# Kernel tuning notes

Hardware: AMD Instinct MI355X
Metric: run time of the kernel (lower is better)

The kernel has to match this reference:

```python
import jax, jax.numpy as jnp
import numpy as np

BATCH = 65536
INPUT_DIM = 256
FIELD_DIM = 32
OUTPUT_DIM = 30


def setup_inputs() -> dict:
    key = jax.random.key(0)
    k1, k2, k3 = jax.random.split(key, 3)
    x = jax.random.normal(k1, (BATCH, INPUT_DIM), dtype=jnp.float32)
    kernel = jax.random.normal(k2, (INPUT_DIM, OUTPUT_DIM), dtype=jnp.float32) * 0.1
    field_weight_matrix = jax.random.normal(k3, (FIELD_DIM, FIELD_DIM), dtype=jnp.float32) * 0.1
    # field_dict[i] = i % FIELD_DIM (matches init_kwargs)
    field_ids = (jnp.arange(INPUT_DIM) % FIELD_DIM).astype(jnp.int32)
    return {"x": x, "kernel": kernel, "field_weight_matrix": field_weight_matrix, "field_ids": field_ids}


def reference(x, kernel, field_weight_matrix, field_ids):
    # Pairwise factor weights: (k_i . k_j) for all i,j  -> [D, D]
    kk = kernel @ kernel.T
    # Field-weight gather: F[field[i], field[j]]  -> [D, D]
    fw = field_weight_matrix[field_ids[:, None], field_ids[None, :]]
    # Only i < j pairs, as in the original double loop
    M = jnp.triu(kk * fw, k=1)
    # out_b = sum_{i<j} x_bi * x_bj * M_ij
    out = jnp.einsum("bi,ij,bj->b", x, M, x)
    return out
```

## Files before the change

### kernel.cpp

```cpp
#include <hip/hip_runtime.h>
#include <stdint.h>
#include <stddef.h>

#define IDIM 256

typedef __attribute__((ext_vector_type(8))) short bf16x8;
typedef __attribute__((ext_vector_type(4))) float f32x4;

__device__ __forceinline__ short f2bf(float f) {
    union { float f; unsigned u; } v; v.f = f;
    unsigned r = v.u + 0x7FFFu + ((v.u >> 16) & 1u);
    return (short)(r >> 16);
}

#define FIOFF 73728
#define FWOFF 74752
#define KOFF  78848
#define LDSZ  95232

#define SWZ(r) ((((r) >> 1) & 3) << 4)

__global__ __launch_bounds__(1024, 4)
void fused_qform(const float* __restrict__ X, const float* __restrict__ K,
                 const float* __restrict__ FW, const int* __restrict__ FI,
                 float* __restrict__ out) {
    __shared__ char lds[LDSZ];
    const int tid  = threadIdx.x;
    const int lane = tid & 63;
    const int wave = tid >> 6;
    const int l15  = lane & 15;
    const int g    = lane >> 4;
    const int wrow = blockIdx.x * 256 + wave * 16;
    const int kbase = g * 8;

    float kv[8];
    {
        const float* kr = K + (size_t)(16 * wave + l15) * 30 + kbase;
        #pragma unroll
        for (int e = 0; e < 8; ++e)
            kv[e] = (kbase + e < 30) ? kr[e] : 0.f;
    }
    if (wave < 4) {
        const char* src = (const char*)FW + wave * 1024 + lane * 16;
        __builtin_amdgcn_global_load_lds(
            (const __attribute__((address_space(1))) unsigned*)src,
            (__attribute__((address_space(3))) unsigned*)(lds + FWOFF + wave * 1024),
            16, 0, 0);
    } else if (wave == 4) {
        const char* src = (const char*)FI + lane * 16;
        __builtin_amdgcn_global_load_lds(
            (const __attribute__((address_space(1))) unsigned*)src,
            (__attribute__((address_space(3))) unsigned*)(lds + FIOFF),
            16, 0, 0);
    }
    __builtin_amdgcn_sched_barrier(0);

    const float* xrow = X + (size_t)(wrow + l15) * IDIM + kbase;
    float4 pa[4], pb[4];
    pa[0] = *(const float4*)(xrow + 0 * 32);
    pb[0] = *(const float4*)(xrow + 0 * 32 + 4);
    pa[1] = *(const float4*)(xrow + 1 * 32);
    pb[1] = *(const float4*)(xrow + 1 * 32 + 4);
    pa[2] = *(const float4*)(xrow + 2 * 32);
    pb[2] = *(const float4*)(xrow + 2 * 32 + 4);
    pa[3] = *(const float4*)(xrow + 3 * 32);
    pb[3] = *(const float4*)(xrow + 3 * 32 + 4);
    __builtin_amdgcn_sched_barrier(0);

    {
        bf16x8 f;
        #pragma unroll
        for (int e = 0; e < 8; ++e) f[e] = f2bf(kv[e]);
        *(bf16x8*)(lds + KOFF + wave * 1024 + lane * 16) = f;
    }
    {
        const int ht = tid >> 7;
        const int r  = (tid >> 3) & 15;
        const int a  = tid & 7;
        const int zb = ((ht * (ht + 1) + (2 * ht + 1)) << 10) + r * 64 + ((a * 4) ^ SWZ(r));
        *(unsigned*)(lds + zb) = 0u;
    }
    asm volatile("s_waitcnt vmcnt(8) lgkmcnt(0)" ::: "memory");
    __builtin_amdgcn_s_barrier();
    asm volatile("" ::: "memory");

    {
        const f32x4 kz = (f32x4){0.f, 0.f, 0.f, 0.f};
        const int* ldsFI = (const int*)(lds + FIOFF);
        const float* ldsFW = (const float*)(lds + FWOFF);

        const int v   = wave >> 1;
        const int par = wave & 1;
        const int tb1 = v;
        const int tb2 = 15 - v;
        const bf16x8 bf1 = *(const bf16x8*)(lds + KOFF + tb1 * 1024 + lane * 16);
        const bf16x8 bf2 = *(const bf16x8*)(lds + KOFF + tb2 * 1024 + lane * 16);
        const int fij1 = ldsFI[16 * tb1 + l15];
        const int fij2 = ldsFI[16 * tb2 + l15];

#define BUILD_TILE(ta, tb, fb, fij) do {                                          \
        const bf16x8 aa = *(const bf16x8*)(lds + KOFF + (ta) * 1024 + lane * 16); \
        f32x4 kk = __builtin_amdgcn_mfma_f32_16x16x32_bf16(aa, fb, kz, 0, 0, 0);  \
        const int tjm = (tb) >> 1;                                                \
        const int mb  = ((tjm * (tjm + 1) + (ta)) << 10);                         \
        const int jb0 = (((tb) & 1) << 5) + 2 * l15;                              \
        const int j   = 16 * (tb) + l15;                                          \
        _Pragma("unroll")                                                         \
        for (int q = 0; q < 4; ++q) {                                             \
            const int i15 = g * 4 + q;                                            \
            const int i   = 16 * (ta) + i15;                                      \
            const float fw = ldsFW[ldsFI[16 * (ta) + i15] * 32 + (fij)];          \
            const float val = (j > i) ? kk[q] * fw : 0.f;                         \
            *(short*)(lds + mb + i15 * 64 + (jb0 ^ SWZ(i15))) = f2bf(val);        \
        }                                                                         \
    } while (0)

        #pragma unroll
        for (int ta = 0; ta < 16; ++ta) {
            if ((ta & 1) == par) {
                if (ta <= tb1) BUILD_TILE(ta, tb1, bf1, fij1);
                if (ta <= tb2) BUILD_TILE(ta, tb2, bf2, fij2);
            }
        }
#undef BUILD_TILE
    }

    asm volatile("s_waitcnt lgkmcnt(0)" ::: "memory");
    __builtin_amdgcn_s_barrier();
    asm volatile("" ::: "memory");

    f32x4 acc[16];
    #pragma unroll
    for (int t = 0; t < 16; ++t) acc[t] = (f32x4){0.f, 0.f, 0.f, 0.f};

    const unsigned laneoff = (unsigned)l15 * 64u + (unsigned)((g * 16) ^ SWZ(l15));

    #pragma unroll
    for (int tj = 0; tj < 8; ++tj) {
        const int s = tj & 3;
        const float4 fa = pa[s], fb = pb[s];
        bf16x8 af;
        af[0] = f2bf(fa.x); af[1] = f2bf(fa.y); af[2] = f2bf(fa.z); af[3] = f2bf(fa.w);
        af[4] = f2bf(fb.x); af[5] = f2bf(fb.y); af[6] = f2bf(fb.z); af[7] = f2bf(fb.w);
        if (tj < 4) {
            pa[s] = *(const float4*)(xrow + (tj + 4) * 32);
            pb[s] = *(const float4*)(xrow + (tj + 4) * 32 + 4);
        }
        #pragma unroll
        for (int ti = 0; ti < 16; ++ti) {
            if (ti <= 2 * tj + 1) {
                const bf16x8 b = *(const bf16x8*)(lds + ((tj * (tj + 1) + ti) << 10) + laneoff);
                acc[ti] = __builtin_amdgcn_mfma_f32_16x16x32_bf16(af, b, acc[ti], 0, 0, 0);
            }
        }
    }

    float psum[4] = {0.f, 0.f, 0.f, 0.f};
    const float* xm = X + (size_t)(wrow + g * 4) * IDIM + l15;
    #pragma unroll
    for (int ti = 0; ti < 16; ++ti) {
        #pragma unroll
        for (int q = 0; q < 4; ++q)
            psum[q] += xm[(size_t)q * IDIM + ti * 16] * acc[ti][q];
    }

    #pragma unroll
    for (int q = 0; q < 4; ++q) {
        float v = psum[q];
        v += __shfl_xor(v, 1, 64);
        v += __shfl_xor(v, 2, 64);
        v += __shfl_xor(v, 4, 64);
        v += __shfl_xor(v, 8, 64);
        psum[q] = v;
    }
    if (l15 == 0) {
        #pragma unroll
        for (int q = 0; q < 4; ++q)
            out[wrow + g * 4 + q] = psum[q];
    }
}

extern "C" void kernel_launch(void* const* d_in, const int* in_sizes, int n_in,
                              void* d_out, int out_size, void* d_ws, size_t ws_size,
                              hipStream_t stream) {
    const float* X  = (const float*)d_in[0];
    const float* K  = (const float*)d_in[1];
    const float* FW = (const float*)d_in[2];
    const int*   FI = (const int*)d_in[3];
    const int batch = in_sizes[0] / IDIM;
    fused_qform<<<dim3(batch / 256), dim3(1024), 0, stream>>>(X, K, FW, FI, (float*)d_out);
}
```

Measured before the change: 108.7 us.

## Halve block size and alias K staging buffer into M tile region

The block shrinks from 1024 to 512 threads covering 128 rows, and the bf16 K staging buffer now aliases the last M tile row instead of having its own region. LDS per block drops so two blocks can share a CU. Building M is reorganised: waves 0-6 build the tiles for columns 0-13, then after an extra barrier each wave builds the column 14/15 tiles from K values already held in registers. The cost is that every block rebuilds the whole M matrix for half as many rows, plus one more barrier.

```diff
diff --git a/kernel.cpp b/kernel.cpp
--- a/kernel.cpp
+++ b/kernel.cpp
@@ -15,12 +15,12 @@
 
 #define FIOFF 73728
 #define FWOFF 74752
-#define KOFF  78848
-#define LDSZ  95232
+#define LDSZ  78848
 
 #define SWZ(r) ((((r) >> 1) & 3) << 4)
-
-__global__ __launch_bounds__(1024, 4)
+#define KBT(t) (lds + (56 + (t)) * 1024 + lane * 16)
+
+__global__ __launch_bounds__(512, 4)
 void fused_qform(const float* __restrict__ X, const float* __restrict__ K,
                  const float* __restrict__ FW, const int* __restrict__ FI,
                  float* __restrict__ out) {
@@ -30,15 +30,18 @@
     const int wave = tid >> 6;
     const int l15  = lane & 15;
     const int g    = lane >> 4;
-    const int wrow = blockIdx.x * 256 + wave * 16;
+    const int wrow = blockIdx.x * 128 + wave * 16;
     const int kbase = g * 8;
 
-    float kv[8];
+    float kv0[8], kv1[8];
     {
-        const float* kr = K + (size_t)(16 * wave + l15) * 30 + kbase;
-        #pragma unroll
-        for (int e = 0; e < 8; ++e)
-            kv[e] = (kbase + e < 30) ? kr[e] : 0.f;
+        const float* kr0 = K + (size_t)(16 * (2 * wave)     + l15) * 30 + kbase;
+        const float* kr1 = K + (size_t)(16 * (2 * wave + 1) + l15) * 30 + kbase;
+        #pragma unroll
+        for (int e = 0; e < 8; ++e) {
+            kv0[e] = (kbase + e < 30) ? kr0[e] : 0.f;
+            kv1[e] = (kbase + e < 30) ? kr1[e] : 0.f;
+        }
     }
     if (wave < 4) {
         const char* src = (const char*)FW + wave * 1024 + lane * 16;
@@ -68,38 +71,30 @@
     __builtin_amdgcn_sched_barrier(0);
 
     {
-        bf16x8 f;
-        #pragma unroll
-        for (int e = 0; e < 8; ++e) f[e] = f2bf(kv[e]);
-        *(bf16x8*)(lds + KOFF + wave * 1024 + lane * 16) = f;
+        bf16x8 f0, f1;
+        #pragma unroll
+        for (int e = 0; e < 8; ++e) { f0[e] = f2bf(kv0[e]); f1[e] = f2bf(kv1[e]); }
+        *(bf16x8*)KBT(2 * wave)     = f0;
+        *(bf16x8*)KBT(2 * wave + 1) = f1;
     }
     {
-        const int ht = tid >> 7;
-        const int r  = (tid >> 3) & 15;
-        const int a  = tid & 7;
-        const int zb = ((ht * (ht + 1) + (2 * ht + 1)) << 10) + r * 64 + ((a * 4) ^ SWZ(r));
-        *(unsigned*)(lds + zb) = 0u;
+        const int ht = tid >> 6;
+        if (ht < 7) {
+            const int r  = (lane >> 2) & 15;
+            const int a  = lane & 3;
+            const int zb = ((ht * (ht + 1) + (2 * ht + 1)) << 10) + r * 64 + ((a * 8) ^ SWZ(r));
+            *(unsigned long long*)(lds + zb) = 0ull;
+        }
     }
     asm volatile("s_waitcnt vmcnt(8) lgkmcnt(0)" ::: "memory");
     __builtin_amdgcn_s_barrier();
     asm volatile("" ::: "memory");
 
-    {
-        const f32x4 kz = (f32x4){0.f, 0.f, 0.f, 0.f};
-        const int* ldsFI = (const int*)(lds + FIOFF);
-        const float* ldsFW = (const float*)(lds + FWOFF);
-
-        const int v   = wave >> 1;
-        const int par = wave & 1;
-        const int tb1 = v;
-        const int tb2 = 15 - v;
-        const bf16x8 bf1 = *(const bf16x8*)(lds + KOFF + tb1 * 1024 + lane * 16);
-        const bf16x8 bf2 = *(const bf16x8*)(lds + KOFF + tb2 * 1024 + lane * 16);
-        const int fij1 = ldsFI[16 * tb1 + l15];
-        const int fij2 = ldsFI[16 * tb2 + l15];
-
-#define BUILD_TILE(ta, tb, fb, fij) do {                                          \
-        const bf16x8 aa = *(const bf16x8*)(lds + KOFF + (ta) * 1024 + lane * 16); \
+    const f32x4 kz = (f32x4){0.f, 0.f, 0.f, 0.f};
+    const int* ldsFI = (const int*)(lds + FIOFF);
+    const float* ldsFW = (const float*)(lds + FWOFF);
+
+#define BUILD_TILE_R(ta, tb, aa, fb, fij) do {                                    \
         f32x4 kk = __builtin_amdgcn_mfma_f32_16x16x32_bf16(aa, fb, kz, 0, 0, 0);  \
         const int tjm = (tb) >> 1;                                                \
         const int mb  = ((tjm * (tjm + 1) + (ta)) << 10);                         \
@@ -114,16 +109,43 @@
             *(short*)(lds + mb + i15 * 64 + (jb0 ^ SWZ(i15))) = f2bf(val);        \
         }                                                                         \
     } while (0)
-
-        #pragma unroll
-        for (int ta = 0; ta < 16; ++ta) {
-            if ((ta & 1) == par) {
-                if (ta <= tb1) BUILD_TILE(ta, tb1, bf1, fij1);
-                if (ta <= tb2) BUILD_TILE(ta, tb2, bf2, fij2);
-            }
-        }
+#define BUILD_TILE(ta, tb, fb, fij) do {                                          \
+        const bf16x8 aa_ = *(const bf16x8*)KBT(ta);                               \
+        BUILD_TILE_R(ta, tb, aa_, fb, fij);                                       \
+    } while (0)
+
+    if (wave < 7) {
+        const int tb1 = wave;
+        const int tb2 = 13 - wave;
+        const bf16x8 bf1 = *(const bf16x8*)KBT(tb1);
+        const bf16x8 bf2 = *(const bf16x8*)KBT(tb2);
+        const int fij1 = ldsFI[16 * tb1 + l15];
+        const int fij2 = ldsFI[16 * tb2 + l15];
+        #pragma unroll
+        for (int ta = 0; ta < 14; ++ta) {
+            if (ta <= tb1) BUILD_TILE(ta, tb1, bf1, fij1);
+            if (ta <= tb2) BUILD_TILE(ta, tb2, bf2, fij2);
+        }
+    }
+
+    const int ta0 = 2 * wave, ta1 = 2 * wave + 1;
+    const bf16x8 fA0 = *(const bf16x8*)KBT(ta0);
+    const bf16x8 fA1 = *(const bf16x8*)KBT(ta1);
+    const bf16x8 fB14 = *(const bf16x8*)KBT(14);
+    const bf16x8 fB15 = *(const bf16x8*)KBT(15);
+    const int fj14 = ldsFI[16 * 14 + l15];
+    const int fj15 = ldsFI[16 * 15 + l15];
+
+    asm volatile("s_waitcnt lgkmcnt(0)" ::: "memory");
+    __builtin_amdgcn_s_barrier();
+    asm volatile("" ::: "memory");
+
+    BUILD_TILE_R(ta0, 14, fA0, fB14, fj14);
+    BUILD_TILE_R(ta0, 15, fA0, fB15, fj15);
+    BUILD_TILE_R(ta1, 14, fA1, fB14, fj14);
+    BUILD_TILE_R(ta1, 15, fA1, fB15, fj15);
 #undef BUILD_TILE
-    }
+#undef BUILD_TILE_R
 
     asm volatile("s_waitcnt lgkmcnt(0)" ::: "memory");
     __builtin_amdgcn_s_barrier();
@@ -188,5 +210,5 @@
     const float* FW = (const float*)d_in[2];
     const int*   FI = (const int*)d_in[3];
     const int batch = in_sizes[0] / IDIM;
-    fused_qform<<<dim3(batch / 256), dim3(1024), 0, stream>>>(X, K, FW, FI, (float*)d_out);
+    fused_qform<<<dim3(batch / 128), dim3(512), 0, stream>>>(X, K, FW, FI, (float*)d_out);
 }
```

Result: no change. 109.3 us (+0.5%).
